# Performance work log

Measured on AMD Instinct MI355X. Metric: run time of the kernel, lower is better.

## Reference

```python
import jax, jax.numpy as jnp
import numpy as np

B, IN_DIM, OUT_DIM, N_KNOTS = 8192, 1024, 1024, 4


def setup_inputs() -> dict:
    key = jax.random.key(0)
    k_feat, k_phase, k_w = jax.random.split(key, 3)
    feats = jax.random.normal(k_feat, (B, IN_DIM), dtype=jnp.float32)
    phase = jax.random.uniform(k_phase, (B, 1), dtype=jnp.float32)  # phase in [0,1)
    x = jnp.concatenate([feats, phase], axis=1)  # [B, IN_DIM+1]
    bound = np.sqrt(6.0 / (OUT_DIM * IN_DIM))
    weight_knots = jax.random.uniform(
        k_w, (N_KNOTS, OUT_DIM, IN_DIM), dtype=jnp.float32, minval=-bound, maxval=bound)
    bias_knots = jnp.zeros((N_KNOTS, OUT_DIM), dtype=jnp.float32)
    return {"x": x, "weight_knots": weight_knots, "bias_knots": bias_knots}


def _cubic(y, mu):
    # Catmull-Rom cubic blend over the 4 gathered knots, y: [B,4,D], mu: [B,1]
    y0, y1, y2, y3 = y[:, 0], y[:, 1], y[:, 2], y[:, 3]
    return ((-0.5 * y0 + 1.5 * y1 - 1.5 * y2 + 0.5 * y3) * mu * mu * mu
            + (y0 - 2.5 * y1 + 2.0 * y2 - 0.5 * y3) * mu * mu
            + (-0.5 * y0 + 0.5 * y2) * mu + y1)


def reference(x, weight_knots, bias_knots):
    K = weight_knots.shape[0]
    phase = x[:, -1]            # [B]
    feats = x[:, :-1]           # [B, IN_DIM]
    pscale = K * phase
    mu = jnp.mod(pscale, 1.0)[:, None]                       # [B, 1]
    i1 = jnp.mod(pscale.astype(jnp.int32), K)
    idx = jnp.stack([jnp.mod(i1 - 1, K), i1,
                     jnp.mod(i1 + 1, K), jnp.mod(i1 + 2, K)], axis=1)  # [B, 4]
    # Exploit linearity: matvec against each knot matrix once, then blend.
    # Mathematically identical to cubic(W0,..,W3) @ feats + cubic(b0,..,b3).
    yk = jnp.einsum('koi,bi->bko', weight_knots, feats)      # [B, K, OUT]
    y4 = jnp.take_along_axis(yk, idx[:, :, None], axis=1)    # [B, 4, OUT]
    b4 = bias_knots[idx]                                     # [B, 4, OUT]
    res = _cubic(y4 + b4, mu)                                # cubic is linear in y
    return jax.nn.elu(res)
```

## Files before the change

kernel.cpp:

```cpp
#include <hip/hip_runtime.h>
#include <math.h>

#define IN_DIM 1024
#define OUT_DIM 1024
#define NROWS 8192
#define XSTRIDE 1025

typedef __attribute__((ext_vector_type(8))) short bf16x8;
typedef __attribute__((ext_vector_type(4))) float f32x4;

static __device__ __forceinline__ unsigned f2bf(float f) {
  union { float f; unsigned u; } v; v.f = f;
  unsigned u = v.u;
  return (u + 0x7fffu + ((u >> 16) & 1u)) >> 16;
}

__global__ __launch_bounds__(256) void prep_kernel(
    const float* __restrict__ x, const float* __restrict__ W,
    unsigned short* __restrict__ Wb, unsigned short* __restrict__ F,
    float* __restrict__ coef)
{
  const int blk = blockIdx.x;
  if (blk < 2048) {
    const int t = blk * 256 + threadIdx.x;
    const int flat = t * 8;
    const int k = flat >> 20;
    const int o = (flat >> 10) & 1023;
    const int i = flat & 1023;
    const float4 fa = *reinterpret_cast<const float4*>(W + flat);
    const float4 fb = *reinterpret_cast<const float4*>(W + flat + 4);
    uint4 pk;
    pk.x = f2bf(fa.x) | (f2bf(fa.y) << 16);
    pk.y = f2bf(fa.z) | (f2bf(fa.w) << 16);
    pk.z = f2bf(fb.x) | (f2bf(fb.y) << 16);
    pk.w = f2bf(fb.z) | (f2bf(fb.w) << 16);
    const int g = (o & 15) | (k << 4) | ((o >> 4) << 6);
    *reinterpret_cast<uint4*>(Wb + (size_t)g * 1024 + i) = pk;
  } else {
    const int b = blk - 2048;
    const float* xr = x + (size_t)b * XSTRIDE;
    const int i = threadIdx.x * 4;
    ushort4 vv;
    vv.x = (unsigned short)f2bf(xr[i]);     vv.y = (unsigned short)f2bf(xr[i + 1]);
    vv.z = (unsigned short)f2bf(xr[i + 2]); vv.w = (unsigned short)f2bf(xr[i + 3]);
    *reinterpret_cast<ushort4*>(F + (size_t)b * 1024 + i) = vv;
    if (threadIdx.x == 0) {
      const float ps = 4.0f * xr[IN_DIM];
      const int ip = (int)ps;
      const int i1 = ip & 3;
      const float mu = ps - (float)ip;
      const float mu2 = mu * mu, mu3 = mu2 * mu;
      const float c0 = -0.5f * mu3 +        mu2 - 0.5f * mu;
      const float c1 =  1.5f * mu3 - 2.5f * mu2 + 1.0f;
      const float c2 = -1.5f * mu3 + 2.0f * mu2 + 0.5f * mu;
      const float c3 =  0.5f * mu3 - 0.5f * mu2;
      const int d0 = (0-i1)&3, d1 = (1-i1)&3, d2 = (2-i1)&3, d3 = (3-i1)&3;
      float4 cv;
      cv.x = d0==0 ? c1 : d0==1 ? c2 : d0==2 ? c3 : c0;
      cv.y = d1==0 ? c1 : d1==1 ? c2 : d1==2 ? c3 : c0;
      cv.z = d2==0 ? c1 : d2==1 ? c2 : d2==2 ? c3 : c0;
      cv.w = d3==0 ? c1 : d3==1 ? c2 : d3==2 ? c3 : c0;
      *reinterpret_cast<float4*>(coef + (size_t)b * 4) = cv;
    }
  }
}

#define BM 256
#define BN 256
#define BK 64

__global__ __launch_bounds__(512, 2) void gemm_kernel(
    const unsigned short* __restrict__ F,
    const unsigned short* __restrict__ Wb,
    const float* __restrict__ coef,
    const float* __restrict__ bias,
    float* __restrict__ out)
{
  __shared__ unsigned short As[2][BM * BK];
  __shared__ unsigned short Bs[2][BN * BK];

  const int tid  = threadIdx.x;
  const int wave = tid >> 6;
  const int lane = tid & 63;
  const int row0  = blockIdx.y * BM;
  const int col0g = blockIdx.x * BN;

  const int srow = tid >> 3;
  const int scc  = tid & 7;
  const int sgc  = (scc ^ (srow & 7)) * 8;

  const int wr = (wave >> 2) * 128;
  const int wc = (wave & 3) * 64;
  const int fm = lane & 15;
  const int fq = lane >> 4;
  const int c0 = ((fq    ) ^ (fm & 7)) * 8;
  const int c1 = ((4 + fq) ^ (fm & 7)) * 8;

  f32x4 acc[8][4];
  const f32x4 zero = {0.f, 0.f, 0.f, 0.f};
  #pragma unroll
  for (int a = 0; a < 8; a++)
    #pragma unroll
    for (int b = 0; b < 4; b++)
      acc[a][b] = zero;

  const unsigned short* Abase = F  + (size_t)row0  * 1024;
  const unsigned short* Bbase = Wb + (size_t)col0g * 1024;

  bf16x8 areg[4][2];
  bf16x8 breg[4][2];

#define STAGE(GB, LDSARR, tile, half) do {                                     \
    _Pragma("unroll")                                                          \
    for (int j_ = 0; j_ < 2; ++j_) {                                           \
      const int r_ = ((half) << 7) + (j_ << 6) + srow;                         \
      __builtin_amdgcn_global_load_lds(                                        \
        (const __attribute__((address_space(1))) void*)(                       \
            (GB) + (size_t)r_ * 1024 + ((tile) << 6) + sgc),                   \
        (__attribute__((address_space(3))) void*)(                             \
            &LDSARR[(tile) & 1][r_ * BK + scc * 8]),                           \
        16, 0, 0);                                                             \
    } } while (0)

#define LDA_QUAD(buf, q)                                                       \
    _Pragma("unroll")                                                          \
    for (int mi_ = 0; mi_ < 4; ++mi_) {                                        \
      const unsigned short* p_ = &As[buf][(wr + (q) * 64 + mi_ * 16 + fm) * BK]; \
      areg[mi_][0] = *reinterpret_cast<const bf16x8*>(p_ + c0);                \
      areg[mi_][1] = *reinterpret_cast<const bf16x8*>(p_ + c1);                \
    }

#define LDB_PAIR(buf, n0)                                                      \
    _Pragma("unroll")                                                          \
    for (int ni_ = 0; ni_ < 2; ++ni_) {                                        \
      const unsigned short* p_ = &Bs[buf][(wc + ((n0) + ni_) * 16 + fm) * BK]; \
      breg[(n0) + ni_][0] = *reinterpret_cast<const bf16x8*>(p_ + c0);         \
      breg[(n0) + ni_][1] = *reinterpret_cast<const bf16x8*>(p_ + c1);         \
    }

#define MFMA_QUAD(q, n0) do {                                                  \
    __builtin_amdgcn_s_setprio(1);                                             \
    _Pragma("unroll")                                                          \
    for (int mi_ = 0; mi_ < 4; ++mi_)                                          \
      _Pragma("unroll")                                                        \
      for (int ni_ = 0; ni_ < 2; ++ni_)                                        \
        _Pragma("unroll")                                                      \
        for (int s_ = 0; s_ < 2; ++s_)                                         \
          acc[(q) * 4 + mi_][(n0) + ni_] =                                     \
              __builtin_amdgcn_mfma_f32_16x16x32_bf16(                         \
                  areg[mi_][s_], breg[(n0) + ni_][s_],                         \
                  acc[(q) * 4 + mi_][(n0) + ni_], 0, 0, 0);                    \
    __builtin_amdgcn_s_setprio(0);                                             \
  } while (0)

#define BAR __builtin_amdgcn_s_barrier()
#define LGKM0 do {                                                             \
    asm volatile("s_waitcnt lgkmcnt(0)" ::: "memory");                         \
    __builtin_amdgcn_sched_barrier(0);                                         \
  } while (0)

  STAGE(Abase, As, 0, 0); STAGE(Abase, As, 0, 1);
  STAGE(Bbase, Bs, 0, 0); STAGE(Bbase, Bs, 0, 1);
  STAGE(Abase, As, 1, 0); STAGE(Abase, As, 1, 1);
  STAGE(Bbase, Bs, 1, 0); STAGE(Bbase, Bs, 1, 1);
  asm volatile("s_waitcnt vmcnt(8)" ::: "memory");
  BAR;

  #pragma unroll 1
  for (int i = 0; i < 8; ++i) {
    const int kt = 2 * i;
    LDA_QUAD(0, 0);
    LDB_PAIR(0, 0);
    if (i >= 1) STAGE(Abase, As, kt + 1, 1);
    BAR; LGKM0; MFMA_QUAD(0, 0); BAR;
    LDB_PAIR(0, 2);
    if (i >= 1) STAGE(Bbase, Bs, kt + 1, 0);
    BAR; LGKM0; MFMA_QUAD(0, 2); BAR;
    LDA_QUAD(0, 1);
    if (i >= 1) STAGE(Bbase, Bs, kt + 1, 1);
    BAR; LGKM0; MFMA_QUAD(1, 2); BAR;
    if (i < 7) { STAGE(Abase, As, kt + 2, 0);
                 asm volatile("s_waitcnt vmcnt(2)" ::: "memory"); }
    else       { asm volatile("s_waitcnt vmcnt(0)" ::: "memory"); }
    BAR; __builtin_amdgcn_sched_barrier(0); MFMA_QUAD(1, 0); BAR;
    LDA_QUAD(1, 0);
    LDB_PAIR(1, 0);
    if (i < 7) STAGE(Abase, As, kt + 2, 1);
    BAR; LGKM0; MFMA_QUAD(0, 0); BAR;
    LDB_PAIR(1, 2);
    if (i < 7) STAGE(Bbase, Bs, kt + 2, 0);
    BAR; LGKM0; MFMA_QUAD(0, 2); BAR;
    LDA_QUAD(1, 1);
    if (i < 7) STAGE(Bbase, Bs, kt + 2, 1);
    BAR; LGKM0; MFMA_QUAD(1, 2); BAR;
    if (i < 7) { STAGE(Abase, As, kt + 3, 0);
                 asm volatile("s_waitcnt vmcnt(2)" ::: "memory"); }
    BAR; __builtin_amdgcn_sched_barrier(0); MFMA_QUAD(1, 0); BAR;
  }

  const int o = fm + 16 * ((col0g + wc) >> 6);
  const float b0 = bias[o];
  const float b1 = bias[OUT_DIM + o];
  const float b2 = bias[2 * OUT_DIM + o];
  const float b3 = bias[3 * OUT_DIM + o];
  #pragma unroll
  for (int mi = 0; mi < 8; ++mi) {
    #pragma unroll
    for (int r = 0; r < 4; ++r) {
      const int rloc = wr + mi * 16 + (fq << 2) + r;
      const float4 c = *reinterpret_cast<const float4*>(coef + (size_t)(row0 + rloc) * 4);
      float v = c.x * (acc[mi][0][r] + b0)
              + c.y * (acc[mi][1][r] + b1)
              + c.z * (acc[mi][2][r] + b2)
              + c.w * (acc[mi][3][r] + b3);
      const float e = __expf(v) - 1.0f;
      v = (v > 0.0f) ? v : e;
      out[(size_t)(row0 + rloc) * OUT_DIM + o] = v;
    }
  }
#undef STAGE
#undef LDA_QUAD
#undef LDB_PAIR
#undef MFMA_QUAD
#undef BAR
#undef LGKM0
}

extern "C" void kernel_launch(void* const* d_in, const int* in_sizes, int n_in,
                              void* d_out, int out_size, void* d_ws, size_t ws_size,
                              hipStream_t stream) {
  const float* x  = (const float*)d_in[0];
  const float* wk = (const float*)d_in[1];
  const float* bk = (const float*)d_in[2];
  float* out = (float*)d_out;

  char* ws = (char*)d_ws;
  unsigned short* Wb = (unsigned short*)ws;
  unsigned short* F  = (unsigned short*)(ws + (8u << 20));
  float* coef        = (float*)(ws + (24u << 20));

  hipLaunchKernelGGL(prep_kernel, dim3(2048 + NROWS), dim3(256), 0, stream,
                     x, wk, Wb, F, coef);
  hipLaunchKernelGGL(gemm_kernel, dim3(4096 / BN, NROWS / BM), dim3(512), 0, stream,
                     F, Wb, coef, bk, out);
}
```

Before: 163.4 us.

## Double-buffer LDS fragment registers to overlap ds_reads with MFMA phases

Splits the A/B fragment registers into separate buffers so LDS reads for the next MFMA phase are issued before or alongside the current phase's MFMAs. The explicit lgkmcnt(0) waits and sched barriers are removed, and the compiler is left to place the waits. This targets the serialization between LDS loads and matrix math in the 8-wave GEMM. The extra fragment registers raise VGPR pressure, and dropping the explicit waits hands scheduling to the compiler, which may insert waits in worse places.

```diff
diff --git a/kernel.cpp b/kernel.cpp
--- a/kernel.cpp
+++ b/kernel.cpp
@@ -107,8 +107,9 @@
   const unsigned short* Abase = F  + (size_t)row0  * 1024;
   const unsigned short* Bbase = Wb + (size_t)col0g * 1024;
 
-  bf16x8 areg[4][2];
-  bf16x8 breg[4][2];
+  bf16x8 A0[4][2], A1[4][2];
+  bf16x8 B01a[2][2], B01b[2][2];
+  bf16x8 B23[2][2];
 
 #define STAGE(GB, LDSARR, tile, half) do {                                     \
     _Pragma("unroll")                                                          \
@@ -122,23 +123,23 @@
         16, 0, 0);                                                             \
     } } while (0)
 
-#define LDA_QUAD(buf, q)                                                       \
+#define DS_A(DST, buf, q)                                                      \
     _Pragma("unroll")                                                          \
     for (int mi_ = 0; mi_ < 4; ++mi_) {                                        \
       const unsigned short* p_ = &As[buf][(wr + (q) * 64 + mi_ * 16 + fm) * BK]; \
-      areg[mi_][0] = *reinterpret_cast<const bf16x8*>(p_ + c0);                \
-      areg[mi_][1] = *reinterpret_cast<const bf16x8*>(p_ + c1);                \
-    }
-
-#define LDB_PAIR(buf, n0)                                                      \
+      DST[mi_][0] = *reinterpret_cast<const bf16x8*>(p_ + c0);                 \
+      DST[mi_][1] = *reinterpret_cast<const bf16x8*>(p_ + c1);                 \
+    }
+
+#define DS_B(DST, buf, n0)                                                     \
     _Pragma("unroll")                                                          \
     for (int ni_ = 0; ni_ < 2; ++ni_) {                                        \
       const unsigned short* p_ = &Bs[buf][(wc + ((n0) + ni_) * 16 + fm) * BK]; \
-      breg[(n0) + ni_][0] = *reinterpret_cast<const bf16x8*>(p_ + c0);         \
-      breg[(n0) + ni_][1] = *reinterpret_cast<const bf16x8*>(p_ + c1);         \
-    }
-
-#define MFMA_QUAD(q, n0) do {                                                  \
+      DST[ni_][0] = *reinterpret_cast<const bf16x8*>(p_ + c0);                 \
+      DST[ni_][1] = *reinterpret_cast<const bf16x8*>(p_ + c1);                 \
+    }
+
+#define MF(q, AR, BR, n0) do {                                                 \
     __builtin_amdgcn_s_setprio(1);                                             \
     _Pragma("unroll")                                                          \
     for (int mi_ = 0; mi_ < 4; ++mi_)                                          \
@@ -148,54 +149,70 @@
         for (int s_ = 0; s_ < 2; ++s_)                                         \
           acc[(q) * 4 + mi_][(n0) + ni_] =                                     \
               __builtin_amdgcn_mfma_f32_16x16x32_bf16(                         \
-                  areg[mi_][s_], breg[(n0) + ni_][s_],                         \
+                  AR[mi_][s_], BR[ni_][s_],                                    \
                   acc[(q) * 4 + mi_][(n0) + ni_], 0, 0, 0);                    \
     __builtin_amdgcn_s_setprio(0);                                             \
   } while (0)
 
 #define BAR __builtin_amdgcn_s_barrier()
-#define LGKM0 do {                                                             \
-    asm volatile("s_waitcnt lgkmcnt(0)" ::: "memory");                         \
-    __builtin_amdgcn_sched_barrier(0);                                         \
-  } while (0)
+#define VMCNT(N) asm volatile("s_waitcnt vmcnt(" #N ")" ::: "memory")
 
   STAGE(Abase, As, 0, 0); STAGE(Abase, As, 0, 1);
   STAGE(Bbase, Bs, 0, 0); STAGE(Bbase, Bs, 0, 1);
   STAGE(Abase, As, 1, 0); STAGE(Abase, As, 1, 1);
   STAGE(Bbase, Bs, 1, 0); STAGE(Bbase, Bs, 1, 1);
-  asm volatile("s_waitcnt vmcnt(8)" ::: "memory");
+  VMCNT(8);
+  DS_A(A0, 0, 0);
+  DS_B(B01a, 0, 0);
   BAR;
 
   #pragma unroll 1
   for (int i = 0; i < 8; ++i) {
     const int kt = 2 * i;
-    LDA_QUAD(0, 0);
-    LDB_PAIR(0, 0);
+    DS_B(B23, 0, 2);
     if (i >= 1) STAGE(Abase, As, kt + 1, 1);
-    BAR; LGKM0; MFMA_QUAD(0, 0); BAR;
-    LDB_PAIR(0, 2);
+    BAR;
+    MF(0, A0, B01a, 0);
+    BAR;
+    DS_A(A1, 0, 1);
     if (i >= 1) STAGE(Bbase, Bs, kt + 1, 0);
-    BAR; LGKM0; MFMA_QUAD(0, 2); BAR;
-    LDA_QUAD(0, 1);
+    BAR;
+    MF(0, A0, B23, 2);
+    BAR;
     if (i >= 1) STAGE(Bbase, Bs, kt + 1, 1);
-    BAR; LGKM0; MFMA_QUAD(1, 2); BAR;
-    if (i < 7) { STAGE(Abase, As, kt + 2, 0);
-                 asm volatile("s_waitcnt vmcnt(2)" ::: "memory"); }
-    else       { asm volatile("s_waitcnt vmcnt(0)" ::: "memory"); }
-    BAR; __builtin_amdgcn_sched_barrier(0); MFMA_QUAD(1, 0); BAR;
-    LDA_QUAD(1, 0);
-    LDB_PAIR(1, 0);
+    BAR;
+    MF(1, A1, B23, 2);
+    BAR;
+    if (i < 7) { STAGE(Abase, As, kt + 2, 0); VMCNT(2); }
+    else        VMCNT(0);
+    DS_A(A0, 1, 0);
+    BAR;
+    MF(1, A1, B01a, 0);
+    DS_B(B01b, 1, 0);
+    BAR;
+    DS_B(B23, 1, 2);
     if (i < 7) STAGE(Abase, As, kt + 2, 1);
-    BAR; LGKM0; MFMA_QUAD(0, 0); BAR;
-    LDB_PAIR(1, 2);
+    BAR;
+    MF(0, A0, B01b, 0);
+    BAR;
+    DS_A(A1, 1, 1);
     if (i < 7) STAGE(Bbase, Bs, kt + 2, 0);
-    BAR; LGKM0; MFMA_QUAD(0, 2); BAR;
-    LDA_QUAD(1, 1);
+    BAR;
+    MF(0, A0, B23, 2);
+    BAR;
     if (i < 7) STAGE(Bbase, Bs, kt + 2, 1);
-    BAR; LGKM0; MFMA_QUAD(1, 2); BAR;
-    if (i < 7) { STAGE(Abase, As, kt + 3, 0);
-                 asm volatile("s_waitcnt vmcnt(2)" ::: "memory"); }
-    BAR; __builtin_amdgcn_sched_barrier(0); MFMA_QUAD(1, 0); BAR;
+    BAR;
+    MF(1, A1, B23, 2);
+    BAR;
+    if (i < 7) {
+      STAGE(Abase, As, kt + 3, 0);
+      VMCNT(2);
+      DS_A(A0, 0, 0);
+    }
+    BAR;
+    MF(1, A1, B01b, 0);
+    if (i < 7) DS_B(B01a, 0, 0);
+    BAR;
   }
 
   const int o = fm + 16 * ((col0g + wc) >> 6);
@@ -219,11 +236,11 @@
     }
   }
 #undef STAGE
-#undef LDA_QUAD
-#undef LDB_PAIR
-#undef MFMA_QUAD
+#undef DS_A
+#undef DS_B
+#undef MF
 #undef BAR
-#undef LGKM0
+#undef VMCNT
 }
 
 extern "C" void kernel_launch(void* const* d_in, const int* in_sizes, int n_in,
```

After: 178.6 us. 9.3% more time.
